# Optimization experiments

Measured on AMD Instinct MI355X. Metric: run time of the kernel, lower is better.

## Reference

```python
import jax, jax.numpy as jnp
import numpy as np
import math

T, B, D, H, DH, DI, V, L = 1024, 4, 512, 8, 64, 2048, 256, 8
STAGES = (2, 4, 2)   # pre, shortened, post layer counts (model_config)
SF = 4               # fixed boundary every SF tokens
S = T // SF          # number of segments


def setup_inputs() -> dict:
    key = jax.random.key(0)
    ks = jax.random.split(key, 12)
    sd = 0.02
    data = jax.random.randint(ks[0], (T, B), 0, V, dtype=jnp.int32)
    t = jnp.arange(T)
    boundaries_gt = jnp.tile(((t % SF) == (SF - 1)).astype(jnp.int32)[:, None], (1, B))
    return {
        'data': data,
        'boundaries_gt': boundaries_gt,
        'word_emb': jax.random.normal(ks[1], (V, D)) * sd,
        'r_w_bias': jax.random.normal(ks[2], (H, DH)) * sd,
        'r_r_bias': jax.random.normal(ks[3], (H, DH)) * sd,
        'null_group': jax.random.normal(ks[4], (1, 1, D)),
        'down_ln_g': jnp.ones((D,), jnp.float32),
        'down_ln_b': jnp.zeros((D,), jnp.float32),
        'qkv_w': jax.random.normal(ks[5], (L, 3 * H * DH, D)) * sd,
        'rk_w': jax.random.normal(ks[6], (L, H * DH, D)) * sd,
        'o_w': jax.random.normal(ks[7], (L, D, H * DH)) * sd,
        'ln1_g': jnp.ones((L, D), jnp.float32),
        'ln1_b': jnp.zeros((L, D), jnp.float32),
        'ff_w1': jax.random.normal(ks[8], (L, DI, D)) * sd,
        'ff_b1': jnp.zeros((L, DI), jnp.float32),
        'ff_w2': jax.random.normal(ks[9], (L, D, DI)) * sd,
        'ff_b2': jnp.zeros((L, D), jnp.float32),
        'ln2_g': jnp.ones((L, D), jnp.float32),
        'ln2_b': jnp.zeros((L, D), jnp.float32),
        'final_w': jax.random.normal(ks[10], (V, D)) * sd,
        'final_b': jnp.zeros((V,), jnp.float32),
    }


def _ln(x, g, b):
    m = jnp.mean(x, -1, keepdims=True)
    v = jnp.mean((x - m) ** 2, -1, keepdims=True)
    return (x - m) * jax.lax.rsqrt(v + 1e-5) * g + b


def _pos_emb(qlen):
    # sinusoidal relative positions qlen-1 .. 0
    pos = jnp.arange(qlen - 1, -1, -1.0, dtype=jnp.float32)
    inv = 1.0 / (10000.0 ** (jnp.arange(0, D, 2, dtype=jnp.float32) / D))
    ang = pos[:, None] * inv[None, :]
    return jnp.concatenate([jnp.sin(ang), jnp.cos(ang)], -1)  # (qlen, D)


def _rel_shift(x):
    # x: (q, k, b, n) -- Transformer-XL relative shift
    q, k, b, n = x.shape
    x = jnp.pad(x, ((0, 0), (1, 0), (0, 0), (0, 0)))
    return x.reshape(k + 1, q, b, n)[1:].reshape(q, k, b, n)


def _stage(x, P, lo, hi, r_w_bias, r_r_bias):
    qkv_w, rk_w, o_w, ln1_g, ln1_b, w1, b1, w2, b2, ln2_g, ln2_b = P
    qlen, bsz, _ = x.shape
    r = _pos_emb(qlen)
    mask = jnp.triu(jnp.ones((qlen, qlen), bool), 1)  # causal
    scale = 1.0 / math.sqrt(DH)
    for i in range(lo, hi):
        h = x @ qkv_w[i].T                                  # (q,b,3HDh)
        qh, kh, vh = jnp.split(h, 3, axis=-1)
        qh = qh.reshape(qlen, bsz, H, DH)
        kh = kh.reshape(qlen, bsz, H, DH)
        vh = vh.reshape(qlen, bsz, H, DH)
        rk = (r @ rk_w[i].T).reshape(qlen, H, DH)
        AC = jnp.einsum('ibnd,jbnd->ijbn', qh + r_w_bias, kh)
        BD = _rel_shift(jnp.einsum('ibnd,jnd->ijbn', qh + r_r_bias, rk))
        score = jnp.where(mask[:, :, None, None], -1e30, (AC + BD) * scale)
        prob = jax.nn.softmax(score, axis=1)
        vec = jnp.einsum('ijbn,jbnd->ibnd', prob, vh).reshape(qlen, bsz, H * DH)
        x = _ln(x + vec @ o_w[i].T, ln1_g[i], ln1_b[i])      # post-LN
        ff = jax.nn.relu(x @ w1[i].T + b1[i]) @ w2[i].T + b2[i]
        x = _ln(x + ff, ln2_g[i], ln2_b[i])
    return x


def _downsample(bnd, hidden, null_group):
    # bnd: (B,T) float, hidden: (T,B,D). Mean-pool each segment, prepend null group.
    seg = jnp.cumsum(bnd, axis=1) - bnd                      # segment id per token
    ind = (seg[:, :, None] == jnp.arange(S, dtype=bnd.dtype)).astype(hidden.dtype)
    w = ind / (ind.sum(axis=1, keepdims=True) + 1e-9)        # (B,T,S)
    short = jnp.einsum('tbd,bts->sbd', hidden, w)
    null = jnp.tile(null_group, (1, hidden.shape[1], 1))
    return jnp.concatenate([null, short], axis=0)            # (S+1,B,D)


def _upsample(bnd, short):
    # token t copies segment cumsum(bnd)[t] (0 == null group)
    seg = jnp.cumsum(bnd, axis=1).astype(jnp.int32)          # (B,T) in [0,S]
    up = jnp.take_along_axis(short, seg.T[:, :, None], axis=0)  # (T,B,D)
    return up / (1.0 + 1e-9)                                 # matches 1/(1+eps) normalizer


def _forward(data, boundaries_gt, word_emb, r_w_bias, r_r_bias, null_group,
             down_ln_g, down_ln_b, qkv_w, rk_w, o_w, ln1_g, ln1_b,
             ff_w1, ff_b1, ff_w2, ff_b2, ln2_g, ln2_b, final_w, final_b):
    P = (qkv_w, rk_w, o_w, ln1_g, ln1_b, ff_w1, ff_b1, ff_w2, ff_b2, ln2_g, ln2_b)
    hidden = word_emb[data]                                  # (T,B,D)
    hidden = _stage(hidden, P, 0, STAGES[0], r_w_bias, r_r_bias)
    residual = hidden
    hard = boundaries_gt.astype(jnp.float32).T               # (B,T)
    short = _downsample(hard, hidden, null_group)
    short = _ln(short, down_ln_g, down_ln_b)
    short = _stage(short, P, STAGES[0], STAGES[0] + STAGES[1], r_w_bias, r_r_bias)
    hidden = _upsample(hard, short) + residual
    hidden = _stage(hidden, P, STAGES[0] + STAGES[1], L, r_w_bias, r_r_bias)
    return hidden @ final_w.T + final_b                      # logits (T,B,V)


def reference(data, boundaries_gt, word_emb, r_w_bias, r_r_bias, null_group,
              down_ln_g, down_ln_b, qkv_w, rk_w, o_w, ln1_g, ln1_b,
              ff_w1, ff_b1, ff_w2, ff_b2, ln2_g, ln2_b, final_w, final_b):
    return _forward(data, boundaries_gt, word_emb, r_w_bias, r_r_bias, null_group,
                    down_ln_g, down_ln_b, qkv_w, rk_w, o_w, ln1_g, ln1_b,
                    ff_w1, ff_b1, ff_w2, ff_b2, ln2_g, ln2_b, final_w, final_b)
```

## Files before the change

### kernel.cpp

```cpp
#include <hip/hip_runtime.h>
#include <math.h>

#define T_  1024
#define B_  4
#define D_  512
#define H_  8
#define DH_ 64
#define DI_ 2048
#define V_  256
#define L_  8
#define S_  256

typedef _Float16 f16;
typedef f16   f16x8 __attribute__((ext_vector_type(8)));
typedef float f32x4 __attribute__((ext_vector_type(4)));

__device__ __forceinline__ void gload16(const void* g, void* l) {
    __builtin_amdgcn_global_load_lds(
        (const __attribute__((address_space(1))) void*)g,
        (__attribute__((address_space(3))) void*)l, 16, 0, 0);
}

__constant__ int cIT[24] = {15,15,14,13,12,11,10,9,8,7,14,6,13,5,12,4,11,3,10,2,9,1,8,0};
__constant__ int cT0[24] = { 0, 8, 0, 0, 0, 0, 0,0,0,0, 8,0, 8,0, 8,0, 8,0, 8,0,8,0,8,0};
__constant__ int cT1[24] = { 8,16, 8, 8, 8, 8, 8,8,8,8,15,7,14,6,13,5,12,4,11,3,10,2,9,1};

__global__ __launch_bounds__(256) void k_f2h(const float* __restrict__ s,
                                             f16* __restrict__ d, int n) {
    int i = (blockIdx.x * 256 + threadIdx.x) * 4;
    int stride = gridDim.x * 1024;
    for (; i < n; i += stride) {
        float4 v = *(const float4*)(s + i);
        d[i + 0] = (f16)v.x; d[i + 1] = (f16)v.y;
        d[i + 2] = (f16)v.z; d[i + 3] = (f16)v.w;
    }
}

__global__ __launch_bounds__(256) void k_embed(const int* __restrict__ data,
                                               const float* __restrict__ emb,
                                               float* __restrict__ x,
                                               f16* __restrict__ xh) {
    int idx = blockIdx.x * 256 + threadIdx.x;
    if (idx >= T_ * B_ * D_) return;
    int d  = idx & (D_ - 1);
    int tb = idx >> 9;
    float v = emb[(size_t)data[tb] * D_ + d];
    x[idx] = v; xh[idx] = (f16)v;
}

__global__ __launch_bounds__(256) void k_posemb(f16* __restrict__ r, int qlen) {
    int p = blockIdx.x;
    int k = threadIdx.x;
    float pos = (float)(qlen - 1 - p);
    float inv = powf(10000.f, -((float)k) / 256.f);
    float ang = pos * inv;
    r[(size_t)p * D_ + k]       = (f16)sinf(ang);
    r[(size_t)p * D_ + 256 + k] = (f16)cosf(ang);
}

template<int BM, int BN, int OUT16, int ACT>
__global__ __launch_bounds__(256) void k_gemm(const f16* __restrict__ X, int lda,
                                              const f16* __restrict__ W,
                                              const float* __restrict__ bias,
                                              void* __restrict__ Yv,
                                              int M, int N, int K) {
    __shared__ f16 As[BM * 64];
    __shared__ f16 Bs[BN * 64];
    const int tid = threadIdx.x, w = tid >> 6, lane = tid & 63;
    const int l16 = lane & 15, lg = lane >> 4;
    int nwg = gridDim.x * gridDim.y;
    int bid = blockIdx.y * gridDim.x + blockIdx.x;
    if ((nwg & 7) == 0) bid = (bid & 7) * (nwg >> 3) + (bid >> 3);
    const int bm = (bid % gridDim.x) * BM, bn = (bid / gridDim.x) * BN;
    const int lrow = lane >> 3, lcol = (lane & 7) * 8;
    constexpr int AI = (BM >= 32) ? BM / 32 : 1;
    constexpr int BI = BN / 32;
    constexpr int MI = (BN == 128) ? 4 : BM / 32;
    constexpr int NJ = 2;
    const int rbase = (BN == 128) ? 0 : (w >> 1) * (BM / 2);
    const int cbase = (BN == 128) ? w * 32 : (w & 1) * 32;
    const f32x4 z4 = {0.f, 0.f, 0.f, 0.f};
    f32x4 acc[MI][NJ];
    #pragma unroll
    for (int i = 0; i < MI; ++i)
        #pragma unroll
        for (int j = 0; j < NJ; ++j) acc[i][j] = z4;

    for (int k0 = 0; k0 < K; k0 += 64) {
        __syncthreads();
        #pragma unroll
        for (int u = 0; u < AI; ++u) {
            int rb = w * (BM / 4) + u * 8;
            gload16(X + (size_t)(bm + rb + lrow) * lda + k0 + lcol, &As[rb * 64]);
        }
        #pragma unroll
        for (int u = 0; u < BI; ++u) {
            int rb = w * (BN / 4) + u * 8;
            gload16(W + (size_t)(bn + rb + lrow) * K + k0 + lcol, &Bs[rb * 64]);
        }
        __syncthreads();
        __builtin_amdgcn_s_setprio(1);
        #pragma unroll
        for (int h = 0; h < 2; ++h) {
            f16x8 af[MI], bf[NJ];
            #pragma unroll
            for (int i = 0; i < MI; ++i)
                af[i] = *(const f16x8*)&As[(rbase + i * 16 + l16) * 64 + h * 32 + lg * 8];
            #pragma unroll
            for (int j = 0; j < NJ; ++j)
                bf[j] = *(const f16x8*)&Bs[(cbase + j * 16 + l16) * 64 + h * 32 + lg * 8];
            #pragma unroll
            for (int i = 0; i < MI; ++i)
                #pragma unroll
                for (int j = 0; j < NJ; ++j)
                    acc[i][j] = __builtin_amdgcn_mfma_f32_16x16x32_f16(af[i], bf[j], acc[i][j], 0, 0, 0);
        }
        __builtin_amdgcn_s_setprio(0);
    }
    #pragma unroll
    for (int i = 0; i < MI; ++i) {
        #pragma unroll
        for (int r = 0; r < 4; ++r) {
            int row = bm + rbase + i * 16 + lg * 4 + r;
            if (row >= M) continue;
            int colb = bn + cbase + l16;
            #pragma unroll
            for (int j = 0; j < NJ; ++j) {
                float v = acc[i][j][r];
                if (bias) v += bias[colb + j * 16];
                if (ACT) v = fmaxf(v, 0.f);
                if (OUT16) ((f16*)Yv)[(size_t)row * N + colb + j * 16] = (f16)v;
                else       ((float*)Yv)[(size_t)row * N + colb + j * 16] = v;
            }
        }
    }
}

__global__ __launch_bounds__(256) void k_ln(float* __restrict__ x,
                                            const float* __restrict__ add,
                                            const float* __restrict__ g,
                                            const float* __restrict__ b,
                                            f16* __restrict__ xh, int rows) {
    int row = blockIdx.x * 4 + (threadIdx.x >> 6);
    if (row >= rows) return;
    int lane = threadIdx.x & 63;
    float* xr = x + (size_t)row * D_ + lane * 8;
    float v[8];
    {
        float4 a0 = *(const float4*)xr;
        float4 a1 = *(const float4*)(xr + 4);
        v[0] = a0.x; v[1] = a0.y; v[2] = a0.z; v[3] = a0.w;
        v[4] = a1.x; v[5] = a1.y; v[6] = a1.z; v[7] = a1.w;
    }
    if (add) {
        const float* ar = add + (size_t)row * D_ + lane * 8;
        float4 a0 = *(const float4*)ar;
        float4 a1 = *(const float4*)(ar + 4);
        v[0] += a0.x; v[1] += a0.y; v[2] += a0.z; v[3] += a0.w;
        v[4] += a1.x; v[5] += a1.y; v[6] += a1.z; v[7] += a1.w;
    }
    float s = 0.f, sq = 0.f;
    #pragma unroll
    for (int u = 0; u < 8; ++u) { s += v[u]; sq += v[u] * v[u]; }
    #pragma unroll
    for (int off = 1; off < 64; off <<= 1) {
        s  += __shfl_xor(s,  off, 64);
        sq += __shfl_xor(sq, off, 64);
    }
    float mean = s * (1.f / (float)D_);
    float var  = sq * (1.f / (float)D_) - mean * mean;
    float rs   = rsqrtf(var + 1e-5f);
    const float* gp = g + lane * 8;
    const float* bp = b + lane * 8;
    float4 g0 = *(const float4*)gp, g1 = *(const float4*)(gp + 4);
    float4 b0 = *(const float4*)bp, b1 = *(const float4*)(bp + 4);
    float gg[8] = {g0.x, g0.y, g0.z, g0.w, g1.x, g1.y, g1.z, g1.w};
    float bb[8] = {b0.x, b0.y, b0.z, b0.w, b1.x, b1.y, b1.z, b1.w};
    float o[8];
    #pragma unroll
    for (int u = 0; u < 8; ++u) o[u] = (v[u] - mean) * rs * gg[u] + bb[u];
    *(float4*)xr       = make_float4(o[0], o[1], o[2], o[3]);
    *(float4*)(xr + 4) = make_float4(o[4], o[5], o[6], o[7]);
    f16x8 hv;
    #pragma unroll
    for (int u = 0; u < 8; ++u) hv[u] = (f16)o[u];
    *(f16x8*)(xh + (size_t)row * D_ + lane * 8) = hv;
}

__global__ __launch_bounds__(256) void k_downln(const float* __restrict__ x,
                                                const float* __restrict__ nullg,
                                                const float* __restrict__ g,
                                                const float* __restrict__ bi,
                                                float* __restrict__ xs,
                                                f16* __restrict__ xsh) {
    int row = blockIdx.x * 4 + (threadIdx.x >> 6);
    if (row >= (S_ + 1) * B_) return;
    int lane = threadIdx.x & 63;
    int s = row >> 2, b = row & 3;
    float v[8];
    if (s == 0) {
        const float* np = nullg + lane * 8;
        float4 a0 = *(const float4*)np, a1 = *(const float4*)(np + 4);
        v[0] = a0.x; v[1] = a0.y; v[2] = a0.z; v[3] = a0.w;
        v[4] = a1.x; v[5] = a1.y; v[6] = a1.z; v[7] = a1.w;
    } else {
        int t0 = (s - 1) * 4;
        #pragma unroll
        for (int u = 0; u < 8; ++u) v[u] = 0.f;
        #pragma unroll
        for (int k = 0; k < 4; ++k) {
            const float* xp = x + ((size_t)(t0 + k) * B_ + b) * D_ + lane * 8;
            float4 a0 = *(const float4*)xp, a1 = *(const float4*)(xp + 4);
            v[0] += a0.x; v[1] += a0.y; v[2] += a0.z; v[3] += a0.w;
            v[4] += a1.x; v[5] += a1.y; v[6] += a1.z; v[7] += a1.w;
        }
        #pragma unroll
        for (int u = 0; u < 8; ++u) v[u] *= 0.25f;
    }
    float sm = 0.f, sq = 0.f;
    #pragma unroll
    for (int u = 0; u < 8; ++u) { sm += v[u]; sq += v[u] * v[u]; }
    #pragma unroll
    for (int off = 1; off < 64; off <<= 1) {
        sm += __shfl_xor(sm, off, 64);
        sq += __shfl_xor(sq, off, 64);
    }
    float mean = sm * (1.f / (float)D_);
    float var  = sq * (1.f / (float)D_) - mean * mean;
    float rs   = rsqrtf(var + 1e-5f);
    float o[8];
    #pragma unroll
    for (int u = 0; u < 8; ++u)
        o[u] = (v[u] - mean) * rs * g[lane * 8 + u] + bi[lane * 8 + u];
    float* xp = xs + (size_t)row * D_ + lane * 8;
    *(float4*)xp       = make_float4(o[0], o[1], o[2], o[3]);
    *(float4*)(xp + 4) = make_float4(o[4], o[5], o[6], o[7]);
    f16x8 hv;
    #pragma unroll
    for (int u = 0; u < 8; ++u) hv[u] = (f16)o[u];
    *(f16x8*)(xsh + (size_t)row * D_ + lane * 8) = hv;
}

__global__ __launch_bounds__(256) void k_up(float* __restrict__ x,
                                            const float* __restrict__ xs,
                                            f16* __restrict__ xh) {
    int idx = blockIdx.x * 256 + threadIdx.x;
    if (idx >= T_ * B_ * D_) return;
    int d  = idx & (D_ - 1);
    int tb = idx >> 9;
    int t = tb >> 2, b = tb & 3;
    int seg = (t + 1) >> 2;
    float v = x[idx] + xs[((size_t)seg * B_ + b) * D_ + d];
    x[idx] = v; xh[idx] = (f16)v;
}

__global__ __launch_bounds__(256) void k_attn(f16* __restrict__ qkv,
                                              const f16* __restrict__ rkb,
                                              int ldr,
                                              const float* __restrict__ rwb,
                                              const float* __restrict__ rrb,
                                              int Q, float* __restrict__ part) {
    __shared__ f16 RKs[192 * 64];
    __shared__ f16 Ks[64 * 64];
    __shared__ f16 Vt[64 * 72];
    __shared__ f16 Pl[4][16 * 72];
    f16* Qw = RKs;
    f16* Qr = RKs + 4096;

    int it, t0, t1, b, n;
    if (Q == 1024) {
        int p = blockIdx.y * gridDim.x + blockIdx.x;
        int xcd = p & 7, qq = p >> 3;
        b = xcd >> 1;
        n = (xcd & 1) * 4 + (qq & 3);
        int slot = qq >> 2;
        it = cIT[slot]; t0 = cT0[slot]; t1 = cT1[slot];
    } else {
        it = gridDim.x - 1 - blockIdx.x;
        b = blockIdx.y >> 3; n = blockIdx.y & 7;
        t0 = 0; t1 = it + 1;
    }
    const int i0 = it * 64;
    const bool partial = (Q == 1024) && (it >= 8);
    const int tid = threadIdx.x, w = tid >> 6, lane = tid & 63;
    const int l16 = lane & 15, lg = lane >> 4;
    const int xsw = (l16 & 7) << 3;
    const int gr8 = lane >> 3;
    const int gsl = ((lane & 7) ^ gr8) * 8;
    const int vjj = tid >> 2, vdb = (tid & 3) * 16;
    const int wb = 48 - w * 16;
    const f32x4 z4 = {0.f, 0.f, 0.f, 0.f};

    {
        int row = tid >> 2, dq = (tid & 3) * 16;
        const f16* qp = qkv + ((size_t)(i0 + row) * B_ + b) * 1536 + n * 64 + dq;
        f16x8 q0 = *(const f16x8*)qp, q1 = *(const f16x8*)(qp + 8);
        int rsw = (row & 7) << 3;
        #pragma unroll
        for (int u = 0; u < 8; ++u) {
            float qa = (float)q0[u], qb2 = (float)q1[u];
            Qw[row * 64 + ((dq + u) ^ rsw)]     = (f16)(qa + rwb[n * 64 + dq + u]);
            Qw[row * 64 + ((dq + 8 + u) ^ rsw)] = (f16)(qb2 + rwb[n * 64 + dq + 8 + u]);
            Qr[row * 64 + ((dq + u) ^ rsw)]     = (f16)(qa + rrb[n * 64 + dq + u]);
            Qr[row * 64 + ((dq + 8 + u) ^ rsw)] = (f16)(qb2 + rrb[n * 64 + dq + 8 + u]);
        }
    }
    __syncthreads();
    f16x8 aqw[2], aqr[2];
    #pragma unroll
    for (int h = 0; h < 2; ++h) {
        aqw[h] = *(const f16x8*)&Qw[(w * 16 + l16) * 64 + ((h * 32 + lg * 8) ^ xsw)];
        aqr[h] = *(const f16x8*)&Qr[(w * 16 + l16) * 64 + ((h * 32 + lg * 8) ^ xsw)];
    }
    __syncthreads();

    const long long pb = (long long)Q - 64 - i0;
    #pragma unroll
    for (int u = 0; u < 4; ++u) {
        int rb = w * 32 + u * 8;
        long long p = pb + t0 * 64 + rb + gr8;
        gload16(rkb + p * ldr + n * 64 + gsl, &RKs[rb * 64]);
    }
    #pragma unroll
    for (int u = 0; u < 2; ++u) {
        int rb = w * 16 + u * 8;
        gload16(qkv + ((size_t)(t0 * 64 + rb + gr8) * B_ + b) * 1536 + 512 + n * 64 + gsl,
                &Ks[rb * 64]);
    }
    f16x8 vr0, vr1;
    {
        const f16* vp = qkv + ((size_t)(t0 * 64 + vjj) * B_ + b) * 1536 + 1024 + n * 64 + vdb;
        vr0 = *(const f16x8*)vp; vr1 = *(const f16x8*)(vp + 8);
    }

    f32x4 acc[4]; acc[0] = z4; acc[1] = z4; acc[2] = z4; acc[3] = z4;
    float psum[4] = {0.f, 0.f, 0.f, 0.f};
    int base = 0;

    for (int t = t0; t < t1; ++t) {
        const int j0 = t * 64;
        __syncthreads();
        #pragma unroll
        for (int u = 0; u < 8; ++u) {
            Vt[(vdb + u) * 72 + (vjj ^ ((u & 7) << 3))]     = vr0[u];
            Vt[(vdb + 8 + u) * 72 + (vjj ^ ((u & 7) << 3))] = vr1[u];
        }
        if (t + 1 < t1) {
            int sb = base + 128; if (sb >= 192) sb -= 192;
            #pragma unroll
            for (int u = 0; u < 2; ++u) {
                int rb = w * 16 + u * 8;
                long long p = pb + j0 + 128 + rb + gr8;
                gload16(rkb + p * ldr + n * 64 + gsl, &RKs[(sb + rb) * 64]);
            }
        }
        f32x4 s1[4]; s1[0] = z4; s1[1] = z4; s1[2] = z4; s1[3] = z4;
        __builtin_amdgcn_s_setprio(1);
        #pragma unroll
        for (int f = 0; f < 4; ++f)
            #pragma unroll
            for (int h = 0; h < 2; ++h) {
                f16x8 bv = *(const f16x8*)&Ks[(f * 16 + l16) * 64 + ((h * 32 + lg * 8) ^ xsw)];
                s1[f] = __builtin_amdgcn_mfma_f32_16x16x32_f16(aqw[h], bv, s1[f], 0, 0, 0);
            }
        __builtin_amdgcn_s_setprio(0);
        if (t + 1 < t1) {
            const f16* vp = qkv + ((size_t)(j0 + 64 + vjj) * B_ + b) * 1536 + 1024 + n * 64 + vdb;
            vr0 = *(const f16x8*)vp; vr1 = *(const f16x8*)(vp + 8);
        }
        f32x4 s2[5]; s2[0] = z4; s2[1] = z4; s2[2] = z4; s2[3] = z4; s2[4] = z4;
        __builtin_amdgcn_s_setprio(1);
        #pragma unroll
        for (int f = 0; f < 5; ++f) {
            int slot = base + wb + f * 16 + l16; if (slot >= 192) slot -= 192;
            #pragma unroll
            for (int h = 0; h < 2; ++h) {
                f16x8 bv = *(const f16x8*)&RKs[slot * 64 + ((h * 32 + lg * 8) ^ xsw)];
                s2[f] = __builtin_amdgcn_mfma_f32_16x16x32_f16(aqr[h], bv, s2[f], 0, 0, 0);
            }
        }
        __builtin_amdgcn_s_setprio(0);
        #pragma unroll
        for (int r = 0; r < 4; ++r) {
            const int q = lg * 4 + r;
            const int iq = i0 + w * 16 + q;
            const int src = (lane & 48) | ((l16 + 15 - q) & 15);
            float g0 = __shfl(s2[0][r], src, 64);
            float g1 = __shfl(s2[1][r], src, 64);
            float g2 = __shfl(s2[2][r], src, 64);
            float g3 = __shfl(s2[3][r], src, 64);
            float g4 = __shfl(s2[4][r], src, 64);
            const bool hi = l16 > q;
            float sv[4];
            sv[0] = (s1[0][r] + (hi ? g1 : g0)) * 0.125f;
            sv[1] = (s1[1][r] + (hi ? g2 : g1)) * 0.125f;
            sv[2] = (s1[2][r] + (hi ? g3 : g2)) * 0.125f;
            sv[3] = (s1[3][r] + (hi ? g4 : g3)) * 0.125f;
            #pragma unroll
            for (int h = 0; h < 4; ++h) {
                int j = j0 + h * 16 + l16;
                if (j > iq || j >= Q) sv[h] = -1e30f;
            }
            float p0 = __expf(sv[0]), p1 = __expf(sv[1]);
            float p2 = __expf(sv[2]), p3 = __expf(sv[3]);
            psum[r] += (p0 + p1) + (p2 + p3);
            Pl[w][q * 72 + l16]      = (f16)p0;
            Pl[w][q * 72 + 16 + l16] = (f16)p1;
            Pl[w][q * 72 + 32 + l16] = (f16)p2;
            Pl[w][q * 72 + 48 + l16] = (f16)p3;
        }
        __syncthreads();
        f16x8 pa0 = *(const f16x8*)&Pl[w][l16 * 72 + lg * 8];
        f16x8 pa1 = *(const f16x8*)&Pl[w][l16 * 72 + 32 + lg * 8];
        __builtin_amdgcn_s_setprio(1);
        #pragma unroll
        for (int f = 0; f < 4; ++f) {
            f16x8 bv0 = *(const f16x8*)&Vt[(f * 16 + l16) * 72 + ((lg * 8) ^ xsw)];
            acc[f] = __builtin_amdgcn_mfma_f32_16x16x32_f16(pa0, bv0, acc[f], 0, 0, 0);
            f16x8 bv1 = *(const f16x8*)&Vt[(f * 16 + l16) * 72 + ((32 + lg * 8) ^ xsw)];
            acc[f] = __builtin_amdgcn_mfma_f32_16x16x32_f16(pa1, bv1, acc[f], 0, 0, 0);
        }
        __builtin_amdgcn_s_setprio(0);
        if (t + 1 < t1) {
            #pragma unroll
            for (int u = 0; u < 2; ++u) {
                int rb = w * 16 + u * 8;
                gload16(qkv + ((size_t)(j0 + 64 + rb + gr8) * B_ + b) * 1536 + 512 + n * 64 + gsl,
                        &Ks[rb * 64]);
            }
        }
        base += 64; if (base >= 192) base -= 192;
    }
    if (partial) {
        int idxp = (b * 8 + n) * 8 + (it - 8);
        float* Pp = part + (size_t)idxp * 8320 + (t0 ? 4160 : 0);
        #pragma unroll
        for (int r = 0; r < 4; ++r) {
            float ps = psum[r];
            ps += __shfl_xor(ps, 1, 64);
            ps += __shfl_xor(ps, 2, 64);
            ps += __shfl_xor(ps, 4, 64);
            ps += __shfl_xor(ps, 8, 64);
            int row = w * 16 + lg * 4 + r;
            #pragma unroll
            for (int f = 0; f < 4; ++f)
                Pp[row * 64 + f * 16 + l16] = acc[f][r];
            if (l16 == 0) Pp[4096 + row] = ps;
        }
    } else {
        #pragma unroll
        for (int r = 0; r < 4; ++r) {
            float ps = psum[r];
            ps += __shfl_xor(ps, 1, 64);
            ps += __shfl_xor(ps, 2, 64);
            ps += __shfl_xor(ps, 4, 64);
            ps += __shfl_xor(ps, 8, 64);
            int i = i0 + w * 16 + lg * 4 + r;
            if (i < Q) {
                float inv = 1.f / ps;
                f16* op = qkv + ((size_t)i * B_ + b) * 1536 + n * 64;
                #pragma unroll
                for (int f = 0; f < 4; ++f)
                    op[f * 16 + l16] = (f16)(acc[f][r] * inv);
            }
        }
    }
}

__global__ __launch_bounds__(256) void k_comb(const float* __restrict__ part,
                                              f16* __restrict__ qkv) {
    int idxp = blockIdx.x;
    int itm = idxp & 7;
    int bn = idxp >> 3;
    int b = bn >> 3, n = bn & 7;
    int i0 = (itm + 8) * 64;
    int row = threadIdx.x >> 2, dp = (threadIdx.x & 3) * 16;
    const float* A  = part + (size_t)idxp * 8320;
    const float* Bp = A + 4160;
    float inv = 1.f / (A[4096 + row] + Bp[4096 + row]);
    f16* op = qkv + ((size_t)(i0 + row) * B_ + b) * 1536 + n * 64 + dp;
    #pragma unroll
    for (int k = 0; k < 16; k += 4) {
        float4 a  = *(const float4*)(A  + row * 64 + dp + k);
        float4 bb = *(const float4*)(Bp + row * 64 + dp + k);
        op[k + 0] = (f16)((a.x + bb.x) * inv);
        op[k + 1] = (f16)((a.y + bb.y) * inv);
        op[k + 2] = (f16)((a.z + bb.z) * inv);
        op[k + 3] = (f16)((a.w + bb.w) * inv);
    }
}

extern "C" void kernel_launch(void* const* d_in, const int* in_sizes, int n_in,
                              void* d_out, int out_size, void* d_ws, size_t ws_size,
                              hipStream_t stream) {
    const int*   data     = (const int*)  d_in[0];
    const float* word_emb = (const float*)d_in[2];
    const float* rwb      = (const float*)d_in[3];
    const float* rrb      = (const float*)d_in[4];
    const float* nullg    = (const float*)d_in[5];
    const float* dg       = (const float*)d_in[6];
    const float* db       = (const float*)d_in[7];
    const float* qkv_w    = (const float*)d_in[8];
    const float* rk_w     = (const float*)d_in[9];
    const float* o_w      = (const float*)d_in[10];
    const float* ln1g     = (const float*)d_in[11];
    const float* ln1b     = (const float*)d_in[12];
    const float* w1       = (const float*)d_in[13];
    const float* b1       = (const float*)d_in[14];
    const float* w2       = (const float*)d_in[15];
    const float* b2       = (const float*)d_in[16];
    const float* ln2g     = (const float*)d_in[17];
    const float* ln2b     = (const float*)d_in[18];
    const float* fw       = (const float*)d_in[19];
    const float* fb       = (const float*)d_in[20];
    float* out = (float*)d_out;
    float* ws  = (float*)d_ws;

    float* x    = ws;
    float* tmp  = x + 2097152;
    float* xs   = tmp + 2097152;
    f16* xh     = (f16*)(xs + 589824);
    f16* xsh    = xh + 2097152;
    f16* r1h    = xsh + 589824;
    f16* r2h    = r1h + 524288;
    f16* rkall  = r2h + 163840;
    f16* bigh   = rkall + 2623488;
    f16* qkv_wh = bigh + 8388608;
    f16* rk_wh  = qkv_wh + 6291456;
    f16* o_wh   = rk_wh + 2097152;
    f16* w1h    = o_wh + 2097152;
    f16* w2h    = w1h + 8388608;
    f16* fwh    = w2h + 8388608;

    auto conv = [&](const float* s, f16* d, int n) {
        int blocks = min(2048, (n + 1023) / 1024);
        k_f2h<<<blocks, 256, 0, stream>>>(s, d, n);
    };
    conv(qkv_w, qkv_wh, L_ * 1536 * 512);
    conv(rk_w,  rk_wh,  L_ * 512 * 512);
    conv(o_w,   o_wh,   L_ * 512 * 512);
    conv(w1,    w1h,    L_ * 2048 * 512);
    conv(w2,    w2h,    L_ * 512 * 2048);
    conv(fw,    fwh,    256 * 512);

    auto gemm = [&](const f16* Xp, int lda, const f16* Wp, const float* bp,
                    void* Yp, int M, int N, int K, int out16, int act) {
        int b64_128 = (N % 128 == 0) ? ((M + 63) / 64) * (N / 128) : 0;
        if (b64_128 >= 768) {
            dim3 g((M + 63) / 64, N / 128);
            if (out16) {
                if (act) k_gemm<64, 128, 1, 1><<<g, 256, 0, stream>>>(Xp, lda, Wp, bp, Yp, M, N, K);
                else     k_gemm<64, 128, 1, 0><<<g, 256, 0, stream>>>(Xp, lda, Wp, bp, Yp, M, N, K);
            } else      k_gemm<64, 128, 0, 0><<<g, 256, 0, stream>>>(Xp, lda, Wp, bp, Yp, M, N, K);
            return;
        }
        int b64_64 = ((M + 63) / 64) * (N / 64);
        if (b64_64 >= 768) {
            dim3 g((M + 63) / 64, N / 64);
            if (out16) {
                if (act) k_gemm<64, 64, 1, 1><<<g, 256, 0, stream>>>(Xp, lda, Wp, bp, Yp, M, N, K);
                else     k_gemm<64, 64, 1, 0><<<g, 256, 0, stream>>>(Xp, lda, Wp, bp, Yp, M, N, K);
            } else      k_gemm<64, 64, 0, 0><<<g, 256, 0, stream>>>(Xp, lda, Wp, bp, Yp, M, N, K);
            return;
        }
        dim3 g((M + 31) / 32, N / 64);
        if (out16) {
            if (act) k_gemm<32, 64, 1, 1><<<g, 256, 0, stream>>>(Xp, lda, Wp, bp, Yp, M, N, K);
            else     k_gemm<32, 64, 1, 0><<<g, 256, 0, stream>>>(Xp, lda, Wp, bp, Yp, M, N, K);
        } else      k_gemm<32, 64, 0, 0><<<g, 256, 0, stream>>>(Xp, lda, Wp, bp, Yp, M, N, K);
    };

    k_embed<<<8192, 256, 0, stream>>>(data, word_emb, x, xh);
    k_posemb<<<1024, 256, 0, stream>>>(r1h, 1024);
    k_posemb<<<257, 256, 0, stream>>>(r2h, 257);

    gemm(r1h, 512, rk_wh,                nullptr, rkall,           1024, 1024, 512, 1, 0);
    gemm(r1h, 512, rk_wh + 6 * 262144,   nullptr, rkall + 1048576, 1024, 1024, 512, 1, 0);
    gemm(r2h, 512, rk_wh + 2 * 262144,   nullptr, rkall + 2097152,  257, 2048, 512, 1, 0);

    auto stage = [&](float* xb, f16* xbh, int Q, int lo, int hi) {
        const int M = Q * B_;
        dim3 gA = (Q == 1024) ? dim3(24, 32) : dim3((Q + 63) / 64, 32);
        dim3 gL((M + 3) / 4);
        for (int i = lo; i < hi; ++i) {
            const f16* rkp; int ldr;
            if (i < 2)       { rkp = rkall + i * 512;                 ldr = 1024; }
            else if (i >= 6) { rkp = rkall + 1048576 + (i - 6) * 512; ldr = 1024; }
            else             { rkp = rkall + 2097152 + (i - 2) * 512; ldr = 2048; }
            gemm(xbh, 512, qkv_wh + (size_t)i * 786432, nullptr, bigh, M, 1536, 512, 1, 0);
            k_attn<<<gA, 256, 0, stream>>>(bigh, rkp, ldr, rwb, rrb, Q, tmp);
            if (Q == 1024) k_comb<<<256, 256, 0, stream>>>(tmp, bigh);
            gemm(bigh, 1536, o_wh + (size_t)i * 262144, nullptr, tmp, M, 512, 512, 0, 0);
            k_ln<<<gL, 256, 0, stream>>>(xb, tmp, ln1g + (size_t)i * 512, ln1b + (size_t)i * 512, xbh, M);
            gemm(xbh, 512, w1h + (size_t)i * 1048576, b1 + (size_t)i * 2048, bigh, M, 2048, 512, 1, 1);
            gemm(bigh, 2048, w2h + (size_t)i * 1048576, b2 + (size_t)i * 512, tmp, M, 512, 2048, 0, 0);
            k_ln<<<gL, 256, 0, stream>>>(xb, tmp, ln2g + (size_t)i * 512, ln2b + (size_t)i * 512, xbh, M);
        }
    };

    stage(x, xh, 1024, 0, 2);
    k_downln<<<257, 256, 0, stream>>>(x, nullg, dg, db, xs, xsh);
    stage(xs, xsh, S_ + 1, 2, 6);
    k_up<<<8192, 256, 0, stream>>>(x, xs, xh);
    stage(x, xh, 1024, 6, 8);
    gemm(xh, 512, fwh, fb, out, T_ * B_, V_, 512, 0, 0);
}
```

Before: 873.2 us.

## Split short-stage attention into balanced partial tiles and store residual GEMM outputs as fp16

The short stage (Q=257) attention is now scheduled through a fixed slot table. Long query tiles are split into two key-range halves whose partial results are merged by k_comb, which gives a balanced 8x32 grid instead of a triangular one. The long-stage slot ordering is also rearranged for better pairing. Separately, the o-projection and FFN2 GEMMs now write fp16 outputs that k_ln reads, halving that traffic. The risk is a small precision loss in the residual add and an extra combine launch in the short stage.

```diff
diff --git a/kernel.cpp b/kernel.cpp
--- a/kernel.cpp
+++ b/kernel.cpp
@@ -21,9 +21,12 @@
         (__attribute__((address_space(3))) void*)l, 16, 0, 0);
 }
 
-__constant__ int cIT[24] = {15,15,14,13,12,11,10,9,8,7,14,6,13,5,12,4,11,3,10,2,9,1,8,0};
-__constant__ int cT0[24] = { 0, 8, 0, 0, 0, 0, 0,0,0,0, 8,0, 8,0, 8,0, 8,0, 8,0,8,0,8,0};
-__constant__ int cT1[24] = { 8,16, 8, 8, 8, 8, 8,8,8,8,15,7,14,6,13,5,12,4,11,3,10,2,9,1};
+__constant__ int cIT[24] = {15,15,14,13,12,11,10, 9,  8, 7,14, 6,13, 5,12, 4,  8, 0, 9, 1,10, 2,11, 3};
+__constant__ int cT0[24] = { 0, 8, 0, 0, 0, 0, 0, 0,  0, 0, 8, 0, 8, 0, 8, 0,  8, 0, 8, 0, 8, 0, 8, 0};
+__constant__ int cT1[24] = { 8,16, 8, 8, 8, 8, 8, 8,  8, 8,15, 7,14, 6,13, 5,  9, 1,10, 2,11, 3,12, 4};
+__constant__ int cIT2[8] = {4,4,3,3,2,2,1,0};
+__constant__ int cT02[8] = {0,3,0,2,0,2,0,0};
+__constant__ int cT12[8] = {3,5,2,4,2,3,2,1};
 
 __global__ __launch_bounds__(256) void k_f2h(const float* __restrict__ s,
                                              f16* __restrict__ d, int n) {
@@ -137,7 +140,7 @@
 }
 
 __global__ __launch_bounds__(256) void k_ln(float* __restrict__ x,
-                                            const float* __restrict__ add,
+                                            const f16* __restrict__ add,
                                             const float* __restrict__ g,
                                             const float* __restrict__ b,
                                             f16* __restrict__ xh, int rows) {
@@ -153,11 +156,9 @@
         v[4] = a1.x; v[5] = a1.y; v[6] = a1.z; v[7] = a1.w;
     }
     if (add) {
-        const float* ar = add + (size_t)row * D_ + lane * 8;
-        float4 a0 = *(const float4*)ar;
-        float4 a1 = *(const float4*)(ar + 4);
-        v[0] += a0.x; v[1] += a0.y; v[2] += a0.z; v[3] += a0.w;
-        v[4] += a1.x; v[5] += a1.y; v[6] += a1.z; v[7] += a1.w;
+        f16x8 a = *(const f16x8*)(add + (size_t)row * D_ + lane * 8);
+        #pragma unroll
+        for (int u = 0; u < 8; ++u) v[u] += (float)a[u];
     }
     float s = 0.f, sq = 0.f;
     #pragma unroll
@@ -268,20 +269,25 @@
     f16* Qr = RKs + 4096;
 
     int it, t0, t1, b, n;
-    if (Q == 1024) {
+    bool partial;
+    int idxp;
+    {
         int p = blockIdx.y * gridDim.x + blockIdx.x;
         int xcd = p & 7, qq = p >> 3;
         b = xcd >> 1;
         n = (xcd & 1) * 4 + (qq & 3);
         int slot = qq >> 2;
-        it = cIT[slot]; t0 = cT0[slot]; t1 = cT1[slot];
-    } else {
-        it = gridDim.x - 1 - blockIdx.x;
-        b = blockIdx.y >> 3; n = blockIdx.y & 7;
-        t0 = 0; t1 = it + 1;
+        if (Q == 1024) {
+            it = cIT[slot]; t0 = cT0[slot]; t1 = cT1[slot];
+            partial = (it >= 8);
+            idxp = (b * 8 + n) * 8 + (it - 8);
+        } else {
+            it = cIT2[slot]; t0 = cT02[slot]; t1 = cT12[slot];
+            partial = (it >= 2);
+            idxp = (b * 8 + n) * 3 + (it - 2);
+        }
     }
     const int i0 = it * 64;
-    const bool partial = (Q == 1024) && (it >= 8);
     const int tid = threadIdx.x, w = tid >> 6, lane = tid & 63;
     const int l16 = lane & 15, lg = lane >> 4;
     const int xsw = (l16 & 7) << 3;
@@ -432,7 +438,6 @@
         base += 64; if (base >= 192) base -= 192;
     }
     if (partial) {
-        int idxp = (b * 8 + n) * 8 + (it - 8);
         float* Pp = part + (size_t)idxp * 8320 + (t0 ? 4160 : 0);
         #pragma unroll
         for (int r = 0; r < 4; ++r) {
@@ -468,13 +473,15 @@
 }
 
 __global__ __launch_bounds__(256) void k_comb(const float* __restrict__ part,
-                                              f16* __restrict__ qkv) {
+                                              f16* __restrict__ qkv,
+                                              int nm, int itbase, int Q) {
     int idxp = blockIdx.x;
-    int itm = idxp & 7;
-    int bn = idxp >> 3;
+    int m = idxp % nm;
+    int bn = idxp / nm;
     int b = bn >> 3, n = bn & 7;
-    int i0 = (itm + 8) * 64;
+    int i0 = (m + itbase) * 64;
     int row = threadIdx.x >> 2, dp = (threadIdx.x & 3) * 16;
+    if (i0 + row >= Q) return;
     const float* A  = part + (size_t)idxp * 8320;
     const float* Bp = A + 4160;
     float inv = 1.f / (A[4096 + row] + Bp[4096 + row]);
@@ -531,6 +538,7 @@
     f16* w1h    = o_wh + 2097152;
     f16* w2h    = w1h + 8388608;
     f16* fwh    = w2h + 8388608;
+    f16* tmph   = (f16*)tmp;
 
     auto conv = [&](const float* s, f16* d, int n) {
         int blocks = min(2048, (n + 1023) / 1024);
@@ -580,7 +588,7 @@
 
     auto stage = [&](float* xb, f16* xbh, int Q, int lo, int hi) {
         const int M = Q * B_;
-        dim3 gA = (Q == 1024) ? dim3(24, 32) : dim3((Q + 63) / 64, 32);
+        dim3 gA = (Q == 1024) ? dim3(24, 32) : dim3(8, 32);
         dim3 gL((M + 3) / 4);
         for (int i = lo; i < hi; ++i) {
             const f16* rkp; int ldr;
@@ -589,12 +597,13 @@
             else             { rkp = rkall + 2097152 + (i - 2) * 512; ldr = 2048; }
             gemm(xbh, 512, qkv_wh + (size_t)i * 786432, nullptr, bigh, M, 1536, 512, 1, 0);
             k_attn<<<gA, 256, 0, stream>>>(bigh, rkp, ldr, rwb, rrb, Q, tmp);
-            if (Q == 1024) k_comb<<<256, 256, 0, stream>>>(tmp, bigh);
-            gemm(bigh, 1536, o_wh + (size_t)i * 262144, nullptr, tmp, M, 512, 512, 0, 0);
-            k_ln<<<gL, 256, 0, stream>>>(xb, tmp, ln1g + (size_t)i * 512, ln1b + (size_t)i * 512, xbh, M);
+            if (Q == 1024) k_comb<<<256, 256, 0, stream>>>(tmp, bigh, 8, 8, 1024);
+            else           k_comb<<<96, 256, 0, stream>>>(tmp, bigh, 3, 2, 257);
+            gemm(bigh, 1536, o_wh + (size_t)i * 262144, nullptr, tmph, M, 512, 512, 1, 0);
+            k_ln<<<gL, 256, 0, stream>>>(xb, tmph, ln1g + (size_t)i * 512, ln1b + (size_t)i * 512, xbh, M);
             gemm(xbh, 512, w1h + (size_t)i * 1048576, b1 + (size_t)i * 2048, bigh, M, 2048, 512, 1, 1);
-            gemm(bigh, 2048, w2h + (size_t)i * 1048576, b2 + (size_t)i * 512, tmp, M, 512, 2048, 0, 0);
-            k_ln<<<gL, 256, 0, stream>>>(xb, tmp, ln2g + (size_t)i * 512, ln2b + (size_t)i * 512, xbh, M);
+            gemm(bigh, 2048, w2h + (size_t)i * 1048576, b2 + (size_t)i * 512, tmph, M, 512, 2048, 1, 0);
+            k_ln<<<gL, 256, 0, stream>>>(xb, tmph, ln2g + (size_t)i * 512, ln2b + (size_t)i * 512, xbh, M);
         }
     };
 
```

Measured after the change: 851.9 us. 1.02x faster.
